# Kernel tuning notes

Measured on AMD Instinct MI355X. Metric: run time of the kernel, lower is better.

Reference implementation:

```python
import jax, jax.numpy as jnp
import numpy as np

HID = 64
IN_DIM = 38
NUM_LAYERS = 4
EPS = 1e-5
SLOPE = 0.01  # LeakyReLU default


def _leaky(x):
    return jnp.where(x >= 0, x, SLOPE * x)


def _batchnorm(x, g, b):
    # training-mode BatchNorm1d: batch statistics, biased variance
    m = jnp.mean(x, axis=0)
    v = jnp.mean((x - m) ** 2, axis=0)
    return (x - m) * jax.lax.rsqrt(v + EPS) * g + b


def _layernorm(x, g, b):
    m = jnp.mean(x, axis=-1, keepdims=True)
    v = jnp.mean((x - m) ** 2, axis=-1, keepdims=True)
    return (x - m) * jax.lax.rsqrt(v + EPS) * g + b


def setup_inputs() -> dict:
    key = jax.random.key(0)
    ks = jax.random.split(key, 12)
    N, E, NG = 100000, 1600000, 128
    edge_index = jax.random.randint(ks[0], (2, E), 0, N)
    n_feats = jax.random.normal(ks[1], (N, IN_DIM), dtype=jnp.float32)
    batch = jnp.sort(jax.random.randint(ks[2], (N,), 0, NG))

    def xavier(k, shape):
        fan_in, fan_out = shape[-2], shape[-1]
        lim = np.sqrt(6.0 / (fan_in + fan_out))
        return jax.random.uniform(k, shape, jnp.float32, -lim, lim)

    return {
        "edge_index": edge_index,
        "n_feats": n_feats,
        "batch": batch,
        "num_graphs": NG,
        "W_enc": xavier(ks[3], (IN_DIM, HID)),
        "b_enc": jnp.zeros((HID,), jnp.float32),
        "bn1_g": jnp.ones((HID,), jnp.float32),
        "bn1_b": jnp.zeros((HID,), jnp.float32),
        "a_w": xavier(ks[4], (NUM_LAYERS, 2 * HID, 1))[..., 0],  # [L, 2H]
        "lin_w": xavier(ks[5], (NUM_LAYERS, HID, HID)),
        "lin_b": jnp.zeros((NUM_LAYERS, HID), jnp.float32),
        "ln_g": jnp.ones((NUM_LAYERS, HID), jnp.float32),
        "ln_b": jnp.zeros((NUM_LAYERS, HID), jnp.float32),
        "bn2_g": jnp.ones((HID,), jnp.float32),
        "bn2_b": jnp.zeros((HID,), jnp.float32),
    }


def _update_v(feat, u, v, aw, lw, lb, lng, lnb):
    N = feat.shape[0]
    u_feat = feat[u]                      # [E, H] gather
    v_feat = feat[v]                      # [E, H] gather
    # attn = Linear([u||v]) with no bias -> split the weight
    attn = u_feat @ aw[:HID] + v_feat @ aw[HID:]      # [E]
    # segment softmax over edges grouped by destination v
    amax = jax.ops.segment_max(attn, v, num_segments=N)  # -inf for empty
    ex = jnp.exp(attn - amax[v])
    denom = jax.ops.segment_sum(ex, v, num_segments=N)
    w = ex / denom[v]                     # [E]
    msg = jax.ops.segment_sum(u_feat * w[:, None], v, num_segments=N)  # [N, H]
    return _leaky(_layernorm(msg @ lw + lb, lng, lnb))


def reference(edge_index, n_feats, batch, num_graphs, W_enc, b_enc, bn1_g, bn1_b,
              a_w, lin_w, lin_b, ln_g, ln_b, bn2_g, bn2_b):
    u, v = edge_index[0], edge_index[1]
    feat = _batchnorm(n_feats @ W_enc + b_enc, bn1_g, bn1_b)  # encoder
    acc = feat
    for l in range(NUM_LAYERS):
        feat = _update_v(feat, u, v, a_w[l], lin_w[l], lin_b[l], ln_g[l], ln_b[l])
        acc = acc + feat
    node_feats = acc / (NUM_LAYERS + 1)   # mean over layer outputs
    # scatter-mean over graphs
    sums = jax.ops.segment_sum(node_feats, batch, num_segments=num_graphs)
    cnts = jax.ops.segment_sum(jnp.ones_like(batch, jnp.float32), batch,
                               num_segments=num_graphs)
    prot = sums / jnp.maximum(cnts, 1.0)[:, None]
    return _leaky(_batchnorm(prot, bn2_g, bn2_b))
```

## Files before the change

kernel.cpp:

```cpp
#include <hip/hip_runtime.h>
#include <hip/hip_bf16.h>

#define HID 64
#define IN_DIM 38
#define NLAYERS 4
#define EPS 1e-5f
#define SLOPE 0.01f
#define ENC_ROWS 128
#define NBUK 256
#define CHUNK 4096

typedef __hip_bfloat16 bf16;
typedef unsigned int u32;
typedef __attribute__((ext_vector_type(8))) short short8;
typedef __attribute__((ext_vector_type(4))) float f32x4;

__device__ __forceinline__ float ldv(const float* p, int i) { return p[i]; }
__device__ __forceinline__ float ldv(const bf16* p, int i) { return __bfloat162float(p[i]); }

__device__ __forceinline__ short bfbits(float f) {
    bf16 h = __float2bfloat16(f);
    return *reinterpret_cast<short*>(&h);
}
__device__ __forceinline__ short ldbf(const bf16* p, int i) { return ((const short*)p)[i]; }
__device__ __forceinline__ short ldbf(const float* p, int i) { return bfbits(p[i]); }

__device__ __forceinline__ bool tag_is_bf16(const void* bn1g) {
    return *((const u32*)bn1g) != 0x3F800000u;
}

__device__ __forceinline__ float wred_sum(float v) {
    #pragma unroll
    for (int m = 32; m > 0; m >>= 1) v += __shfl_xor(v, m, 64);
    return v;
}

__device__ __forceinline__ float bflo(u32 w) { return __uint_as_float(w << 16); }
__device__ __forceinline__ float bfhi(u32 w) { return __uint_as_float(w & 0xFFFF0000u); }

__device__ __forceinline__ int bucket_of(int v, int N) {
    return (int)(((long long)v * NBUK) / N);
}

template <typename T>
__device__ __forceinline__ void encoder_body(int blk, const T* x, const T* W, const T* bias,
                                             int N, float* enc, float* bnsum, float* bnsq,
                                             float* sx, float* ls, float* lq) {
    int t = threadIdx.x;
    int lane = t & 63;
    int wid = t >> 6;
    int base = blk * ENC_ROWS;
    int rows = min(ENC_ROWS, N - base);
    int total = rows * IN_DIM;
    for (int i = t; i < total; i += 256) sx[i] = ldv(x, base * IN_DIM + i);
    __syncthreads();

    float Wc[IN_DIM];
    #pragma unroll
    for (int k = 0; k < IN_DIM; k++) Wc[k] = ldv(W, k * 64 + lane);
    float bi = ldv(bias, lane);

    float s = 0.f, sq = 0.f;
    for (int r = wid * 32; r < wid * 32 + 32; r++) {
        int n = base + r;
        if (n >= N) break;
        float o = bi;
        #pragma unroll
        for (int k = 0; k < IN_DIM; k++) o += sx[r * IN_DIM + k] * Wc[k];
        enc[(size_t)n * 64 + lane] = o;
        s += o;
        sq += o * o;
    }
    if (t < 64) { ls[t] = 0.f; lq[t] = 0.f; }
    __syncthreads();
    atomicAdd(&ls[lane], s);
    atomicAdd(&lq[lane], sq);
    __syncthreads();
    if (t < 64) {
        atomicAdd(&bnsum[t], ls[t]);
        atomicAdd(&bnsq[t], lq[t]);
    }
}

__global__ __launch_bounds__(256) void k_pre1(const int* __restrict__ ev, int E, int N,
                                              int* __restrict__ bcnt, const void* x, const void* W,
                                              const void* bias, const void* tag, float* enc,
                                              float* bnsum, float* bnsq, int pb) {
    __shared__ float sx[ENC_ROWS * IN_DIM];
    __shared__ float ls[64], lq[64];
    if ((int)blockIdx.x < pb) {
        int* h = (int*)sx;
        h[threadIdx.x] = 0;
        __syncthreads();
        int base = blockIdx.x * CHUNK;
        int end = min(base + CHUNK, E);
        for (int i = base + threadIdx.x; i < end; i += 256) atomicAdd(&h[bucket_of(ev[i], N)], 1);
        __syncthreads();
        int c = h[threadIdx.x];
        if (c) atomicAdd(&bcnt[threadIdx.x], c);
    } else {
        int blk = blockIdx.x - pb;
        if (tag_is_bf16(tag))
            encoder_body<bf16>(blk, (const bf16*)x, (const bf16*)W, (const bf16*)bias, N, enc,
                               bnsum, bnsq, sx, ls, lq);
        else
            encoder_body<float>(blk, (const float*)x, (const float*)W, (const float*)bias, N, enc,
                                bnsum, bnsq, sx, ls, lq);
    }
}

__global__ __launch_bounds__(256) void k_pre2(const int* __restrict__ bcnt, int* __restrict__ bbase,
                                              int* __restrict__ bcur, const float* __restrict__ bnsum,
                                              const float* __restrict__ bnsq, int N,
                                              float* __restrict__ bn1m, float* __restrict__ bn1r) {
    __shared__ int sm[NBUK];
    if (blockIdx.x == 0) {
        int t = threadIdx.x;
        int c = bcnt[t];
        sm[t] = c;
        __syncthreads();
        for (int ofs = 1; ofs < NBUK; ofs <<= 1) {
            int x = (t >= ofs) ? sm[t - ofs] : 0;
            __syncthreads();
            sm[t] += x;
            __syncthreads();
        }
        int excl = sm[t] - c;
        bbase[t] = excl;
        bcur[t] = excl;
        if (t == NBUK - 1) bbase[NBUK] = sm[t];
    } else {
        int h = threadIdx.x;
        if (h < 64) {
            float m = bnsum[h] / (float)N;
            float v = bnsq[h] / (float)N - m * m;
            bn1m[h] = m;
            bn1r[h] = rsqrtf(v + EPS);
        }
    }
}

template <typename T>
__device__ __forceinline__ void bnapply_body(int blk, const float* enc, const float* bn1m,
                                             const float* bn1r, const T* g, const T* b,
                                             const T* aw0, int N, bf16* feat, float* exp_s) {
    int idx = blk * 256 + threadIdx.x;
    int lane = threadIdx.x & 63;
    int n = idx >> 6;
    if (n >= N) return;
    float f = (enc[idx] - bn1m[lane]) * bn1r[lane] * ldv(g, lane) + ldv(b, lane);
    feat[idx] = __float2bfloat16(f);
    float s = wred_sum(f * ldv(aw0, lane));
    if (lane == 0) exp_s[n] = __expf(s);
}

__global__ __launch_bounds__(256) void k_pre3(const int* __restrict__ eu,
                                              const int* __restrict__ ev, int E, int N,
                                              int* __restrict__ bcur, uint2* __restrict__ rec,
                                              const float* enc, const float* bn1m,
                                              const float* bn1r, const void* g, const void* b,
                                              const void* aw0, const void* tag, bf16* feat0,
                                              float* exp_s, int pb) {
    __shared__ int h[NBUK];
    if ((int)blockIdx.x < pb) {
        int t = threadIdx.x;
        h[t] = 0;
        __syncthreads();
        int base = blockIdx.x * CHUNK;
        int end = min(base + CHUNK, E);
        for (int i = base + t; i < end; i += 256) atomicAdd(&h[bucket_of(ev[i], N)], 1);
        __syncthreads();
        int c = h[t];
        int rb = c ? atomicAdd(&bcur[t], c) : 0;
        __syncthreads();
        h[t] = rb;
        __syncthreads();
        for (int i = base + t; i < end; i += 256) {
            int u = eu[i], v = ev[i];
            int pos = atomicAdd(&h[bucket_of(v, N)], 1);
            rec[pos] = make_uint2((u32)u, (u32)v);
        }
    } else {
        int blk = blockIdx.x - pb;
        if (tag_is_bf16(tag))
            bnapply_body<bf16>(blk, enc, bn1m, bn1r, (const bf16*)g, (const bf16*)b,
                               (const bf16*)aw0, N, feat0, exp_s);
        else
            bnapply_body<float>(blk, enc, bn1m, bn1r, (const float*)g, (const float*)b,
                                (const float*)aw0, N, feat0, exp_s);
    }
}

__global__ __launch_bounds__(512) void k_csr(const uint2* __restrict__ rec,
                                             const int* __restrict__ bbase, int N, int E,
                                             int* __restrict__ row_ptr, int* __restrict__ col_u) {
    __shared__ int cnt[512], sc[512];
    int b = blockIdx.x;
    int t = threadIdx.x;
    int lo = (int)(((long long)b * N + NBUK - 1) / NBUK);
    int hi = (int)(((long long)(b + 1) * N + NBUK - 1) / NBUK);
    if (hi > N) hi = N;
    int nn = hi - lo;
    cnt[t] = 0;
    __syncthreads();
    int rlo = bbase[b], rhi = bbase[b + 1];
    for (int i = rlo + t; i < rhi; i += 512) atomicAdd(&cnt[(int)rec[i].y - lo], 1);
    __syncthreads();
    int c = cnt[t];
    sc[t] = c;
    __syncthreads();
    for (int ofs = 1; ofs < 512; ofs <<= 1) {
        int x = (t >= ofs) ? sc[t - ofs] : 0;
        __syncthreads();
        sc[t] += x;
        __syncthreads();
    }
    int excl = sc[t] - c;
    if (t < nn) row_ptr[lo + t] = rlo + excl;
    cnt[t] = rlo + excl;
    __syncthreads();
    for (int i = rlo + t; i < rhi; i += 512) {
        uint2 r = rec[i];
        int pos = atomicAdd(&cnt[(int)r.y - lo], 1);
        col_u[pos] = (int)r.x;
    }
    if (b == NBUK - 1 && t == 0) row_ptr[N] = E;
}

template <typename T>
__device__ __forceinline__ void layer_body(const int* __restrict__ row_ptr,
                                           const int* __restrict__ col_u,
                                           const float* __restrict__ exp_s,
                                           const bf16* __restrict__ feat, const T* lw, const T* lb,
                                           const T* lng, const T* lnb, const T* aw_next, int N,
                                           bf16* feat_out, float* exp_s_next,
                                           uint2 (*s_ue)[2][32], short* smsg, float (*ps)[4],
                                           float (*pq)[4], float (*pe)[4], float* mrs) {
    int lane = threadIdx.x & 63;
    int w = threadIdx.x >> 6;
    int half = lane >> 5;
    int h = lane & 31;
    int g = h >> 3;
    int cq = h & 7;
    int n0 = blockIdx.x * 16;

    #pragma unroll 1
    for (int it = 0; it < 2; it++) {
        int nl = w * 4 + it * 2 + half;
        int n = n0 + nl;
        int st = 0, en = 0;
        if (n < N) { st = row_ptr[n]; en = row_ptr[n + 1]; }
        float macc[8];
        #pragma unroll
        for (int x = 0; x < 8; x++) macc[x] = 0.f;
        float den = 0.f;

        for (int j0 = st; j0 < en; j0 += 32) {
            int jj = j0 + h;
            u32 uu = 0;
            float ee = 0.f;
            if (jj < en) {
                uu = (u32)col_u[jj];
                ee = exp_s[uu];
            }
            den += ee;
            s_ue[w][half][h] = make_uint2(uu, __float_as_uint(ee));
            int cnt = en - j0;
            if (cnt > 32) cnt = 32;
            int ng4 = (cnt + 3) >> 2;
            uint4 fv[8];
            float e4[8];
            #pragma unroll
            for (int k = 0; k < 8; k++) {
                if (k < ng4) {
                    uint2 ue = s_ue[w][half][k * 4 + g];
                    e4[k] = __uint_as_float(ue.y);
                    fv[k] = *(const uint4*)(feat + ((size_t)ue.x << 6) + (cq << 3));
                }
            }
            #pragma unroll
            for (int k = 0; k < 8; k++) {
                if (k < ng4) {
                    float e = e4[k];
                    macc[0] += e * bflo(fv[k].x);
                    macc[1] += e * bfhi(fv[k].x);
                    macc[2] += e * bflo(fv[k].y);
                    macc[3] += e * bfhi(fv[k].y);
                    macc[4] += e * bflo(fv[k].z);
                    macc[5] += e * bfhi(fv[k].z);
                    macc[6] += e * bflo(fv[k].w);
                    macc[7] += e * bfhi(fv[k].w);
                }
            }
        }

        #pragma unroll
        for (int m = 8; m <= 16; m <<= 1) {
            #pragma unroll
            for (int x = 0; x < 8; x++) macc[x] += __shfl_xor(macc[x], m, 64);
        }
        #pragma unroll
        for (int m = 1; m <= 16; m <<= 1) den += __shfl_xor(den, m, 64);
        float inv = (den > 0.f) ? 1.f / den : 0.f;
        if (g == 0) {
            short8 sv;
            #pragma unroll
            for (int x = 0; x < 8; x++) sv[x] = bfbits(macc[x] * inv);
            *(short8*)(smsg + nl * 72 + cq * 8) = sv;
        }
    }
    __syncthreads();

    int l15 = lane & 15;
    int q = lane >> 4;
    int col = w * 16 + l15;

    short8 bf0, bf1;
    #pragma unroll
    for (int j = 0; j < 8; j++) {
        bf0[j] = ldbf(lw, (q * 8 + j) * 64 + col);
        bf1[j] = ldbf(lw, (32 + q * 8 + j) * 64 + col);
    }
    short8 af0 = *(const short8*)(smsg + l15 * 72 + q * 8);
    short8 af1 = *(const short8*)(smsg + l15 * 72 + 32 + q * 8);
    float lbv = ldv(lb, col);
    f32x4 c = {lbv, lbv, lbv, lbv};
    c = __builtin_amdgcn_mfma_f32_16x16x32_bf16(af0, bf0, c, 0, 0, 0);
    c = __builtin_amdgcn_mfma_f32_16x16x32_bf16(af1, bf1, c, 0, 0, 0);

    float o[4], s1[4], s2[4];
    #pragma unroll
    for (int r = 0; r < 4; r++) {
        o[r] = c[r];
        s1[r] = o[r];
        s2[r] = o[r] * o[r];
    }
    #pragma unroll
    for (int m = 1; m <= 8; m <<= 1) {
        #pragma unroll
        for (int r = 0; r < 4; r++) {
            s1[r] += __shfl_xor(s1[r], m, 64);
            s2[r] += __shfl_xor(s2[r], m, 64);
        }
    }
    if (l15 == 0) {
        #pragma unroll
        for (int r = 0; r < 4; r++) {
            ps[q * 4 + r][w] = s1[r];
            pq[q * 4 + r][w] = s2[r];
        }
    }
    __syncthreads();
    if (threadIdx.x < 16) {
        int t = threadIdx.x;
        float S = ps[t][0] + ps[t][1] + ps[t][2] + ps[t][3];
        float Q = pq[t][0] + pq[t][1] + pq[t][2] + pq[t][3];
        float m = S * (1.f / 64.f);
        float var = Q * (1.f / 64.f) - m * m;
        mrs[t] = m;
        mrs[16 + t] = rsqrtf(var + EPS);
    }
    __syncthreads();

    float gcol = ldv(lng, col), bcol = ldv(lnb, col), awv = ldv(aw_next, col);
    float pexp[4];
    #pragma unroll
    for (int r = 0; r < 4; r++) {
        int row = q * 4 + r;
        int n = n0 + row;
        float y = (o[r] - mrs[row]) * mrs[16 + row] * gcol + bcol;
        y = (y >= 0.f) ? y : SLOPE * y;
        if (n < N) feat_out[n * 64 + col] = __float2bfloat16(y);
        pexp[r] = y * awv;
    }
    #pragma unroll
    for (int m = 1; m <= 8; m <<= 1) {
        #pragma unroll
        for (int r = 0; r < 4; r++) pexp[r] += __shfl_xor(pexp[r], m, 64);
    }
    if (l15 == 0) {
        #pragma unroll
        for (int r = 0; r < 4; r++) pe[q * 4 + r][w] = pexp[r];
    }
    __syncthreads();
    if (threadIdx.x < 16) {
        int t = threadIdx.x;
        int n = n0 + t;
        if (n < N) exp_s_next[n] = __expf(pe[t][0] + pe[t][1] + pe[t][2] + pe[t][3]);
    }
}

__global__ __launch_bounds__(256) void k_layer_off(const int* row_ptr, const int* col_u,
                                                   const float* exp_s, const bf16* feat,
                                                   const void* lw, const void* lb, const void* lng,
                                                   const void* lnb, const void* aw, const void* tag,
                                                   int lw_e, int v_e, int aw_e, int N,
                                                   bf16* feat_out, float* exp_s_next) {
    __shared__ uint2 s_ue[4][2][32];
    __shared__ short smsg[16 * 72];
    __shared__ float ps[16][4], pq[16][4], pe[16][4], mrs[32];
    if (tag_is_bf16(tag))
        layer_body<bf16>(row_ptr, col_u, exp_s, feat, (const bf16*)lw + lw_e, (const bf16*)lb + v_e,
                         (const bf16*)lng + v_e, (const bf16*)lnb + v_e, (const bf16*)aw + aw_e, N,
                         feat_out, exp_s_next, s_ue, smsg, ps, pq, pe, mrs);
    else
        layer_body<float>(row_ptr, col_u, exp_s, feat, (const float*)lw + lw_e,
                          (const float*)lb + v_e, (const float*)lng + v_e, (const float*)lnb + v_e,
                          (const float*)aw + aw_e, N, feat_out, exp_s_next, s_ue, smsg, ps, pq, pe,
                          mrs);
}

__global__ __launch_bounds__(256) void k_pool(const bf16* __restrict__ f0,
                                              const bf16* __restrict__ f1,
                                              const bf16* __restrict__ f2,
                                              const bf16* __restrict__ f3,
                                              const bf16* __restrict__ f4,
                                              const int* __restrict__ batch, int N,
                                              float* __restrict__ gsum, float* __restrict__ gcnt) {
    int lane = threadIdx.x & 63;
    int wave = blockIdx.x * 4 + (threadIdx.x >> 6);
    int n0 = wave * 64;
    if (n0 >= N) return;
    int nend = min(n0 + 64, N);
    float run = 0.f, cnt = 0.f;
    int cur = batch[n0];
    for (int n = n0; n < nend; n++) {
        int g = batch[n];
        int idx = n * 64 + lane;
        float v = (__bfloat162float(f0[idx]) + __bfloat162float(f1[idx]) +
                   __bfloat162float(f2[idx]) + __bfloat162float(f3[idx]) +
                   __bfloat162float(f4[idx])) *
                  (1.0f / (NLAYERS + 1));
        if (g != cur) {
            atomicAdd(&gsum[cur * 64 + lane], run);
            if (lane == 0) atomicAdd(&gcnt[cur], cnt);
            run = 0.f;
            cnt = 0.f;
            cur = g;
        }
        run += v;
        cnt += 1.f;
    }
    atomicAdd(&gsum[cur * 64 + lane], run);
    if (lane == 0) atomicAdd(&gcnt[cur], cnt);
}

template <typename T>
__device__ __forceinline__ void final_body(const float* gsum, const float* gcnt, int NG,
                                           const T* g2, const T* b2, T* out, float (*ps)[64],
                                           float (*pq)[64], float* stats) {
    int t = threadIdx.x;
    int h = t & 63;
    int p = t >> 6;
    float s = 0.f, q = 0.f;
    #pragma unroll 4
    for (int i = p; i < NG; i += 4) {
        float c = fmaxf(gcnt[i], 1.f);
        float v = gsum[i * 64 + h] / c;
        s += v;
        q += v * v;
    }
    ps[p][h] = s;
    pq[p][h] = q;
    __syncthreads();
    if (t < 64) {
        float S = ps[0][t] + ps[1][t] + ps[2][t] + ps[3][t];
        float Q = pq[0][t] + pq[1][t] + pq[2][t] + pq[3][t];
        float m = S / (float)NG;
        float var = Q / (float)NG - m * m;
        stats[t] = m;
        stats[64 + t] = rsqrtf(var + EPS);
    }
    __syncthreads();
    float m = stats[h];
    float r = stats[64 + h];
    float gg = ldv(g2, h), bb = ldv(b2, h);
    for (int i = p; i < NG; i += 4) {
        float c = fmaxf(gcnt[i], 1.f);
        float v = gsum[i * 64 + h] / c;
        float y = (v - m) * r * gg + bb;
        y = (y >= 0.f) ? y : SLOPE * y;
        out[i * 64 + h] = (T)y;
    }
}

__global__ __launch_bounds__(256) void k_final(const float* gsum, const float* gcnt, int NG,
                                               const void* g2, const void* b2, const void* tag,
                                               void* out) {
    __shared__ float ps[4][64], pq[4][64], stats[128];
    if (tag_is_bf16(tag))
        final_body<bf16>(gsum, gcnt, NG, (const bf16*)g2, (const bf16*)b2, (bf16*)out, ps, pq,
                         stats);
    else
        final_body<float>(gsum, gcnt, NG, (const float*)g2, (const float*)b2, (float*)out, ps, pq,
                          stats);
}

extern "C" void kernel_launch(void* const* d_in, const int* in_sizes, int n_in, void* d_out,
                              int out_size, void* d_ws, size_t ws_size, hipStream_t stream) {
    const int* edge_index = (const int*)d_in[0];
    const void* n_feats = d_in[1];
    const int* batch = (const int*)d_in[2];
    const void* W_enc = d_in[4];
    const void* b_enc = d_in[5];
    const void* bn1_g = d_in[6];
    const void* bn1_b = d_in[7];
    const void* a_w = d_in[8];
    const void* lin_w = d_in[9];
    const void* lin_b = d_in[10];
    const void* ln_g = d_in[11];
    const void* ln_b = d_in[12];
    const void* bn2_g = d_in[13];
    const void* bn2_b = d_in[14];

    const int E = in_sizes[0] / 2;
    const int N = in_sizes[1] / IN_DIM;
    const int NG = out_size / HID;
    const int* eu = edge_index;
    const int* ev = edge_index + E;

    char* base = (char*)d_ws;
    size_t off = 0;
    auto alloc = [&](size_t bytes) -> void* {
        void* p = base + off;
        off = (off + bytes + 255) & ~(size_t)255;
        return p;
    };
    int* bcnt = (int*)alloc(NBUK * 4);
    float* gsum = (float*)alloc((size_t)NG * 64 * 4);
    float* gcnt = (float*)alloc((size_t)NG * 4);
    float* bnsum = (float*)alloc(64 * 4);
    float* bnsq = (float*)alloc(64 * 4);
    size_t zbytes = off;
    int* bbase = (int*)alloc((NBUK + 1) * 4);
    int* bcur = (int*)alloc(NBUK * 4);
    int* row_ptr = (int*)alloc((size_t)(N + 1) * 4);
    int* col_u = (int*)alloc((size_t)E * 4);
    uint2* rec = (uint2*)alloc((size_t)E * 8);
    bf16* featbase = (bf16*)alloc((size_t)N * 64 * 2 * 5);
    float* eA = (float*)alloc((size_t)N * 4);
    float* eB = (float*)alloc((size_t)N * 4);
    float* bn1m = (float*)alloc(64 * 4);
    float* bn1r = (float*)alloc(64 * 4);
    (void)ws_size;

    bf16* feats[5];
    for (int l = 0; l < 5; l++) feats[l] = featbase + (size_t)l * N * 64;
    float* enc = (float*)feats[3];

    hipMemsetAsync(d_ws, 0, zbytes, stream);

    const int pb = (E + CHUNK - 1) / CHUNK;
    const int encB = (N + ENC_ROWS - 1) / ENC_ROWS;
    const int bnapB = (N * 64 + 255) / 256;

    k_pre1<<<pb + encB, 256, 0, stream>>>(ev, E, N, bcnt, n_feats, W_enc, b_enc, bn1_g, enc,
                                          bnsum, bnsq, pb);
    k_pre2<<<2, 256, 0, stream>>>(bcnt, bbase, bcur, bnsum, bnsq, N, bn1m, bn1r);
    k_pre3<<<pb + bnapB, 256, 0, stream>>>(eu, ev, E, N, bcur, rec, enc, bn1m, bn1r, bn1_g,
                                           bn1_b, a_w, bn1_g, feats[0], eA, pb);
    k_csr<<<NBUK, 512, 0, stream>>>(rec, bbase, N, E, row_ptr, col_u);

    float* ein = eA;
    float* eout = eB;
    for (int l = 0; l < NLAYERS; l++) {
        int lnext = (l + 1) & 3;
        k_layer_off<<<(N + 15) / 16, 256, 0, stream>>>(row_ptr, col_u, ein, feats[l], lin_w, lin_b,
                                                       ln_g, ln_b, a_w, bn1_g,
                                                        l * HID * HID,
                                                        l * HID,
                                                        lnext * 2 * HID, N, feats[l + 1],
                                                       eout);
        float* te = ein; ein = eout; eout = te;
    }

    int pw = (N + 63) / 64;
    k_pool<<<(pw + 3) / 4, 256, 0, stream>>>(feats[0], feats[1], feats[2], feats[3], feats[4],
                                             batch, N, gsum, gcnt);
    k_final<<<1, 256, 0, stream>>>(gsum, gcnt, NG, bn2_g, bn2_b, bn1_g, d_out);
}
```

Measured before the change: 420.9 us.

## Sort destination nodes by in-degree within buckets for balanced layer work

The CSR build now groups nodes inside each bucket by in-degree (a 64-bin histogram and scan) and emits per-slot (start,end) ranges plus a permutation to the original node id. The layer kernel processes nodes in this degree-sorted order, so half-waves that share a loop handle similar edge counts, which cuts divergence and tail imbalance. In exchange the feature and exp gathers and writes become scattered through the permutation, which loses locality on the output stores.

```diff
diff --git a/kernel.cpp b/kernel.cpp
--- a/kernel.cpp
+++ b/kernel.cpp
@@ -193,8 +193,10 @@
 
 __global__ __launch_bounds__(512) void k_csr(const uint2* __restrict__ rec,
                                              const int* __restrict__ bbase, int N, int E,
-                                             int* __restrict__ row_ptr, int* __restrict__ col_u) {
+                                             int2* __restrict__ rse, int* __restrict__ perm,
+                                             int* __restrict__ col_u) {
     __shared__ int cnt[512], sc[512];
+    __shared__ int dh[64];
     int b = blockIdx.x;
     int t = threadIdx.x;
     int lo = (int)(((long long)b * N + NBUK - 1) / NBUK);
@@ -215,27 +217,50 @@
         sc[t] += x;
         __syncthreads();
     }
-    int excl = sc[t] - c;
-    if (t < nn) row_ptr[lo + t] = rlo + excl;
-    cnt[t] = rlo + excl;
+    int estart = rlo + sc[t] - c;
+    cnt[t] = estart;
     __syncthreads();
     for (int i = rlo + t; i < rhi; i += 512) {
         uint2 r = rec[i];
         int pos = atomicAdd(&cnt[(int)r.y - lo], 1);
         col_u[pos] = (int)r.x;
     }
-    if (b == NBUK - 1 && t == 0) row_ptr[N] = E;
+
+    if (t < 64) dh[t] = 0;
+    __syncthreads();
+    int db = min(c, 63);
+    if (t < nn) atomicAdd(&dh[db], 1);
+    __syncthreads();
+    if (t < 64) {
+        int orig = dh[t];
+        int v = orig;
+        #pragma unroll
+        for (int ofs = 1; ofs < 64; ofs <<= 1) {
+            int x = __shfl_up(v, ofs, 64);
+            if (t >= ofs) v += x;
+        }
+        dh[t] = v - orig;
+    }
+    __syncthreads();
+    if (t < nn) {
+        int pos = atomicAdd(&dh[db], 1);
+        int sp = lo + pos;
+        rse[sp] = make_int2(estart, estart + c);
+        perm[sp] = lo + t;
+    }
 }
 
 template <typename T>
-__device__ __forceinline__ void layer_body(const int* __restrict__ row_ptr,
+__device__ __forceinline__ void layer_body(const int2* __restrict__ rse,
+                                           const int* __restrict__ perm,
                                            const int* __restrict__ col_u,
                                            const float* __restrict__ exp_s,
                                            const bf16* __restrict__ feat, const T* lw, const T* lb,
                                            const T* lng, const T* lnb, const T* aw_next, int N,
                                            bf16* feat_out, float* exp_s_next,
-                                           uint2 (*s_ue)[2][32], short* smsg, float (*ps)[4],
-                                           float (*pq)[4], float (*pe)[4], float* mrs) {
+                                           uint2 (*s_ue)[2][32], short* smsg, int* spn,
+                                           float (*ps)[4], float (*pq)[4], float (*pe)[4],
+                                           float* mrs) {
     int lane = threadIdx.x & 63;
     int w = threadIdx.x >> 6;
     int half = lane >> 5;
@@ -247,9 +272,14 @@
     #pragma unroll 1
     for (int it = 0; it < 2; it++) {
         int nl = w * 4 + it * 2 + half;
-        int n = n0 + nl;
+        int gi = n0 + nl;
         int st = 0, en = 0;
-        if (n < N) { st = row_ptr[n]; en = row_ptr[n + 1]; }
+        if (gi < N) {
+            int2 se = rse[gi];
+            st = se.x;
+            en = se.y;
+        }
+        if (h == 0) spn[nl] = (gi < N) ? perm[gi] : -1;
         float macc[8];
         #pragma unroll
         for (int x = 0; x < 8; x++) macc[x] = 0.f;
@@ -367,10 +397,10 @@
     #pragma unroll
     for (int r = 0; r < 4; r++) {
         int row = q * 4 + r;
-        int n = n0 + row;
+        int n = spn[row];
         float y = (o[r] - mrs[row]) * mrs[16 + row] * gcol + bcol;
         y = (y >= 0.f) ? y : SLOPE * y;
-        if (n < N) feat_out[n * 64 + col] = __float2bfloat16(y);
+        if (n >= 0) feat_out[n * 64 + col] = __float2bfloat16(y);
         pexp[r] = y * awv;
     }
     #pragma unroll
@@ -385,29 +415,31 @@
     __syncthreads();
     if (threadIdx.x < 16) {
         int t = threadIdx.x;
-        int n = n0 + t;
-        if (n < N) exp_s_next[n] = __expf(pe[t][0] + pe[t][1] + pe[t][2] + pe[t][3]);
-    }
-}
-
-__global__ __launch_bounds__(256) void k_layer_off(const int* row_ptr, const int* col_u,
-                                                   const float* exp_s, const bf16* feat,
-                                                   const void* lw, const void* lb, const void* lng,
-                                                   const void* lnb, const void* aw, const void* tag,
-                                                   int lw_e, int v_e, int aw_e, int N,
-                                                   bf16* feat_out, float* exp_s_next) {
+        int n = spn[t];
+        if (n >= 0) exp_s_next[n] = __expf(pe[t][0] + pe[t][1] + pe[t][2] + pe[t][3]);
+    }
+}
+
+__global__ __launch_bounds__(256) void k_layer_off(const int2* rse, const int* perm,
+                                                   const int* col_u, const float* exp_s,
+                                                   const bf16* feat, const void* lw, const void* lb,
+                                                   const void* lng, const void* lnb, const void* aw,
+                                                   const void* tag, int lw_e, int v_e, int aw_e,
+                                                   int N, bf16* feat_out, float* exp_s_next) {
     __shared__ uint2 s_ue[4][2][32];
     __shared__ short smsg[16 * 72];
+    __shared__ int spn[16];
     __shared__ float ps[16][4], pq[16][4], pe[16][4], mrs[32];
     if (tag_is_bf16(tag))
-        layer_body<bf16>(row_ptr, col_u, exp_s, feat, (const bf16*)lw + lw_e, (const bf16*)lb + v_e,
-                         (const bf16*)lng + v_e, (const bf16*)lnb + v_e, (const bf16*)aw + aw_e, N,
-                         feat_out, exp_s_next, s_ue, smsg, ps, pq, pe, mrs);
+        layer_body<bf16>(rse, perm, col_u, exp_s, feat, (const bf16*)lw + lw_e,
+                         (const bf16*)lb + v_e, (const bf16*)lng + v_e, (const bf16*)lnb + v_e,
+                         (const bf16*)aw + aw_e, N, feat_out, exp_s_next, s_ue, smsg, spn, ps, pq,
+                         pe, mrs);
     else
-        layer_body<float>(row_ptr, col_u, exp_s, feat, (const float*)lw + lw_e,
+        layer_body<float>(rse, perm, col_u, exp_s, feat, (const float*)lw + lw_e,
                           (const float*)lb + v_e, (const float*)lng + v_e, (const float*)lnb + v_e,
-                          (const float*)aw + aw_e, N, feat_out, exp_s_next, s_ue, smsg, ps, pq, pe,
-                          mrs);
+                          (const float*)aw + aw_e, N, feat_out, exp_s_next, s_ue, smsg, spn, ps, pq,
+                          pe, mrs);
 }
 
 __global__ __launch_bounds__(256) void k_pool(const bf16* __restrict__ f0,
@@ -534,7 +566,8 @@
     size_t zbytes = off;
     int* bbase = (int*)alloc((NBUK + 1) * 4);
     int* bcur = (int*)alloc(NBUK * 4);
-    int* row_ptr = (int*)alloc((size_t)(N + 1) * 4);
+    int2* rse = (int2*)alloc((size_t)N * 8);
+    int* perm = (int*)alloc((size_t)N * 4);
     int* col_u = (int*)alloc((size_t)E * 4);
     uint2* rec = (uint2*)alloc((size_t)E * 8);
     bf16* featbase = (bf16*)alloc((size_t)N * 64 * 2 * 5);
@@ -559,14 +592,14 @@
     k_pre2<<<2, 256, 0, stream>>>(bcnt, bbase, bcur, bnsum, bnsq, N, bn1m, bn1r);
     k_pre3<<<pb + bnapB, 256, 0, stream>>>(eu, ev, E, N, bcur, rec, enc, bn1m, bn1r, bn1_g,
                                            bn1_b, a_w, bn1_g, feats[0], eA, pb);
-    k_csr<<<NBUK, 512, 0, stream>>>(rec, bbase, N, E, row_ptr, col_u);
+    k_csr<<<NBUK, 512, 0, stream>>>(rec, bbase, N, E, rse, perm, col_u);
 
     float* ein = eA;
     float* eout = eB;
     for (int l = 0; l < NLAYERS; l++) {
         int lnext = (l + 1) & 3;
-        k_layer_off<<<(N + 15) / 16, 256, 0, stream>>>(row_ptr, col_u, ein, feats[l], lin_w, lin_b,
-                                                       ln_g, ln_b, a_w, bn1_g,
+        k_layer_off<<<(N + 15) / 16, 256, 0, stream>>>(rse, perm, col_u, ein, feats[l], lin_w,
+                                                       lin_b, ln_g, ln_b, a_w, bn1_g,
                                                         l * HID * HID,
                                                         l * HID,
                                                         lnext * 2 * HID, N, feats[l + 1],
```

Result: no change. 427.4 us (+1.5%).
